# Kernel tuning notes

Hardware: AMD Instinct MI355X
Metric: run time of the kernel (lower is better)

The kernel has to match this reference:

```python
import jax, jax.numpy as jnp
import numpy as np

B, W, L, J, I, O = 512, 1024, 64, 8, 32, 128


def setup_inputs() -> dict:
    key = jax.random.key(0)
    ks = jax.random.split(key, 9)
    wm = jax.random.normal(ks[0], (B, W, L), dtype=jnp.float32)
    constants = jax.random.uniform(ks[1], (J, L), minval=-1.0, maxval=1.0, dtype=jnp.float32)
    gammas = jax.random.uniform(ks[2], (J, L), minval=0.0, maxval=1.0, dtype=jnp.float32)
    body_w = jax.random.normal(ks[3], (J, I, L), dtype=jnp.float32) / np.sqrt(L).astype(np.float32)
    body_b = jax.random.normal(ks[4], (J, I), dtype=jnp.float32) * 0.01
    slot_w = jax.random.normal(ks[5], (J, L * I, L), dtype=jnp.float32) / np.sqrt(L).astype(np.float32)
    slot_b = jax.random.normal(ks[6], (J, L * I), dtype=jnp.float32) * 0.01
    head_w = jax.random.normal(ks[7], (O, I), dtype=jnp.float32) / np.sqrt(I).astype(np.float32)
    head_b = jax.random.normal(ks[8], (O,), dtype=jnp.float32) * 0.01
    return {"working_memory": wm, "constants": constants, "gammas": gammas,
            "body_w": body_w, "body_b": body_b, "slot_w": slot_w, "slot_b": slot_b,
            "head_w": head_w, "head_b": head_b}


def reference(working_memory, constants, gammas, body_w, body_b, slot_w, slot_b, head_w, head_b):
    temperature = 1.0
    g = jnp.clip(gammas, 0.0, 1.0)            # (J,L), torch.clamp equivalent
    w1 = 1.0 - g                               # per-element weight (1-gamma)
    # match_scores[j,b,w] = sum_l w1[j,l] * (c[j,l] - wm[b,w,l])^2, expanded to
    # avoid materializing a (J,B,W,L) intermediate:
    A = jnp.sum(w1 * constants * constants, axis=1)                      # (J,)
    cross = jnp.einsum('jl,bwl->jbw', w1 * constants, working_memory)    # (J,B,W)
    quad = jnp.einsum('jl,bwl->jbw', w1, working_memory * working_memory)
    scores = A[:, None, None] - 2.0 * cross + quad                       # (J,B,W)
    attn = jax.nn.softmax(-scores / temperature, axis=-1)                # (J,B,W)
    best = jnp.einsum('jbw,bwl->jbl', attn, working_memory)              # (J,B,L)
    total_mq = jnp.sum(attn * scores, axis=-1).sum(axis=0)               # (B,)
    # body: per-premise Linear(L->I), scaled by mean clamped gamma
    captured = jnp.einsum('jbl,jil->jbi', best, body_w) + body_b[:, None, :]
    g_avg = g.mean(axis=1)                                               # (J,)
    captured_vars = jnp.einsum('j,jbi->bi', g_avg, captured)             # (B,I)
    # slot selector: per-premise Linear(L -> L*I), softmax over slots,
    # scatter best_props values into slots (the original inner l-loop).
    slot_logits = jnp.einsum('jbl,jkl->jbk', best, slot_w) + slot_b[:, None, :]
    slot_probs = jax.nn.softmax(slot_logits.reshape(J, -1, L, I), axis=-1)
    captured_vars = captured_vars + jnp.einsum('jbli,jbl->bi', slot_probs, best)
    output = captured_vars @ head_w.T + head_b                           # (B,O)
    confidence = jnp.exp(-total_mq)[:, None]                             # (B,1)
    return confidence * output
```

## Files before the change

### kernel.cpp

```cpp
#include <hip/hip_runtime.h>
#include <cstdint>
#include <cstddef>

#define B_ 512
#define W_ 1024
#define L_ 64
#define J_ 8
#define I_ 32
#define O_ 128


__global__ __launch_bounds__(64) void k0_prep(const float* __restrict__ constants,
    const float* __restrict__ gammas, float* __restrict__ wcg,
    float* __restrict__ w1g, float* __restrict__ Ag)
{
  const int l = threadIdx.x;
  #pragma unroll
  for (int j = 0; j < J_; ++j) {
    float g = gammas[j*L_ + l];
    g = fminf(fmaxf(g, 0.f), 1.f);
    float c = constants[j*L_ + l];
    float w1 = 1.f - g;
    w1g[j*L_ + l] = w1;
    wcg[j*L_ + l] = w1 * c;
  }
  if (l < J_) {
    float a = 0.f;
    for (int c = 0; c < L_; ++c) {
      float g = gammas[l*L_ + c];
      g = fminf(fmaxf(g, 0.f), 1.f);
      float cc = constants[l*L_ + c];
      a += (1.f - g) * cc * cc;
    }
    Ag[l] = a;
  }
}

__global__ __launch_bounds__(256, 4) void k12_fused(const float* __restrict__ wm,
    const float* __restrict__ wcg, const float* __restrict__ w1g,
    const float* __restrict__ Ag, float* __restrict__ bpart, float* __restrict__ stats)
{
  __shared__ __align__(16) float xs[128 * 68];
  __shared__ __align__(16) float es[J_ * 128];
  __shared__ float redA[4][4], redB[4][4];
  __shared__ float bcast[J_];

  const int tid = threadIdx.x;
  const int b = blockIdx.x, h = blockIdx.y;
  const int lane = tid & 63, wv = tid >> 6;
  const int w = tid & 127;
  const int jh = tid >> 7;
  const int jbase = __builtin_amdgcn_readfirstlane(jh << 2);
  const int lq = tid & 15, wsl = tid >> 4;

  float accb[J_][4];
  #pragma unroll
  for (int j = 0; j < J_; ++j)
    #pragma unroll
    for (int q = 0; q < 4; ++q) accb[j][q] = 0.f;
  float esum[4], msum[4], m0[4];
  #pragma unroll
  for (int jj = 0; jj < 4; ++jj) { esum[jj] = 0.f; msum[jj] = 0.f; }

  const float* wmb = wm + (size_t)b * (W_*L_) + (size_t)h * (512*L_);

  for (int ch = 0; ch < 4; ++ch) {
    __syncthreads();
    const float4* src = (const float4*)(wmb + ch * (128*L_));
    #pragma unroll
    for (int k = 0; k < 8; ++k) {
      int f = k*256 + tid;
      float4 v = src[f];
      int rw = f >> 4, lw = f & 15;
      *(float4*)&xs[rw*68 + lw*4] = v;
    }
    __syncthreads();

    float a1[4], a2[4];
    #pragma unroll
    for (int jj = 0; jj < 4; ++jj) { a1[jj] = 0.f; a2[jj] = 0.f; }
    #pragma unroll
    for (int c = 0; c < 16; ++c) {
      float4 x = *(const float4*)&xs[w*68 + c*4];
      float4 xq;
      xq.x = x.x*x.x; xq.y = x.y*x.y; xq.z = x.z*x.z; xq.w = x.w*x.w;
      #pragma unroll
      for (int jj = 0; jj < 4; ++jj) {
        float4 wc4 = *(const float4*)(wcg + (jbase+jj)*L_ + c*4);
        float4 w14 = *(const float4*)(w1g + (jbase+jj)*L_ + c*4);
        a1[jj] = fmaf(wc4.x, x.x, a1[jj]);
        a1[jj] = fmaf(wc4.y, x.y, a1[jj]);
        a1[jj] = fmaf(wc4.z, x.z, a1[jj]);
        a1[jj] = fmaf(wc4.w, x.w, a1[jj]);
        a2[jj] = fmaf(w14.x, xq.x, a2[jj]);
        a2[jj] = fmaf(w14.y, xq.y, a2[jj]);
        a2[jj] = fmaf(w14.z, xq.z, a2[jj]);
        a2[jj] = fmaf(w14.w, xq.w, a2[jj]);
      }
    }
    float s[4];
    #pragma unroll
    for (int jj = 0; jj < 4; ++jj)
      s[jj] = Ag[jbase+jj] - 2.f*a1[jj] + a2[jj];

    if (ch == 0) {
      #pragma unroll
      for (int jj = 0; jj < 4; ++jj) {
        float mn = s[jj];
        #pragma unroll
        for (int off = 1; off < 64; off <<= 1)
          mn = fminf(mn, __shfl_xor(mn, off));
        if (lane == 0) redA[wv][jj] = mn;
      }
      __syncthreads();
      if (tid < J_) {
        int jj = tid & 3;
        bcast[tid] = (tid < 4) ? fminf(redA[0][jj], redA[1][jj])
                               : fminf(redA[2][jj], redA[3][jj]);
      }
      __syncthreads();
      #pragma unroll
      for (int jj = 0; jj < 4; ++jj) m0[jj] = bcast[jbase+jj];
    }

    #pragma unroll
    for (int jj = 0; jj < 4; ++jj) {
      float e = __expf(m0[jj] - s[jj]);
      esum[jj] += e;
      msum[jj] = fmaf(e, s[jj], msum[jj]);
      es[(jbase+jj)*128 + w] = e;
    }
    __syncthreads();

    #pragma unroll
    for (int tg = 0; tg < 2; ++tg) {
      float4 e4[J_];
      #pragma unroll
      for (int j = 0; j < J_; ++j)
        e4[j] = *(const float4*)&es[j*128 + wsl*8 + tg*4];
      #pragma unroll
      for (int t = 0; t < 4; ++t) {
        int w2 = wsl*8 + tg*4 + t;
        float4 x = *(const float4*)&xs[w2*68 + lq*4];
        #pragma unroll
        for (int j = 0; j < J_; ++j) {
          float ej = (t == 0) ? e4[j].x : (t == 1) ? e4[j].y
                   : (t == 2) ? e4[j].z : e4[j].w;
          accb[j][0] = fmaf(ej, x.x, accb[j][0]);
          accb[j][1] = fmaf(ej, x.y, accb[j][1]);
          accb[j][2] = fmaf(ej, x.z, accb[j][2]);
          accb[j][3] = fmaf(ej, x.w, accb[j][3]);
        }
      }
    }
  }

  #pragma unroll
  for (int jj = 0; jj < 4; ++jj) {
    float e = esum[jj], m = msum[jj];
    #pragma unroll
    for (int off = 1; off < 64; off <<= 1) {
      e += __shfl_xor(e, off);
      m += __shfl_xor(m, off);
    }
    if (lane == 0) { redA[wv][jj] = e; redB[wv][jj] = m; }
  }
  __syncthreads();
  if (tid < J_) {
    int jj = tid & 3;
    float E = (tid < 4) ? redA[0][jj] + redA[1][jj] : redA[2][jj] + redA[3][jj];
    float M = (tid < 4) ? redB[0][jj] + redB[1][jj] : redB[2][jj] + redB[3][jj];
    float* st = stats + (((size_t)h*B_ + b)*J_ + tid)*4;
    st[0] = bcast[tid]; st[1] = E; st[2] = M;
  }

  #pragma unroll
  for (int j = 0; j < J_; ++j)
    *(float4*)&xs[((wsl*J_ + j)*16 + lq)*4] = *(float4*)accb[j];
  __syncthreads();
  if (tid < J_*16) {
    int j = tid >> 4, q = tid & 15;
    float4 sum = make_float4(0.f, 0.f, 0.f, 0.f);
    #pragma unroll
    for (int s2 = 0; s2 < 16; ++s2) {
      float4 p = *(const float4*)&xs[((s2*J_ + j)*16 + q)*4];
      sum.x += p.x; sum.y += p.y; sum.z += p.z; sum.w += p.w;
    }
    *(float4*)&bpart[(((size_t)h*J_ + j)*B_ + b)*L_ + q*4] = sum;
  }
}

__global__ __launch_bounds__(128) void k2b_combine(const float* __restrict__ bpart,
    const float* __restrict__ stats, float* __restrict__ best, float* __restrict__ conf)
{
  __shared__ float mred[J_];
  const int b = blockIdx.x, tid = threadIdx.x;
  const int j = tid >> 4, q = tid & 15;
  const float* st0 = stats + ((size_t)b*J_ + j)*4;
  const float* st1 = stats + (((size_t)B_ + b)*J_ + j)*4;
  float m0a = st0[0], E0 = st0[1], M0 = st0[2];
  float m0b = st1[0], E1 = st1[1], M1 = st1[2];
  float M = fminf(m0a, m0b);
  float s0 = __expf(M - m0a), s1 = __expf(M - m0b);
  float E = s0*E0 + s1*E1;
  float inv = 1.f / E;
  float4 p0 = *(const float4*)&bpart[((size_t)j*B_ + b)*L_ + q*4];
  float4 p1 = *(const float4*)&bpart[(((size_t)J_ + j)*B_ + b)*L_ + q*4];
  float4 o;
  o.x = (s0*p0.x + s1*p1.x) * inv;
  o.y = (s0*p0.y + s1*p1.y) * inv;
  o.z = (s0*p0.z + s1*p1.z) * inv;
  o.w = (s0*p0.w + s1*p1.w) * inv;
  *(float4*)&best[((size_t)j*B_ + b)*L_ + q*4] = o;
  if (q == 0) mred[j] = (s0*M0 + s1*M1) * inv;
  __syncthreads();
  if (tid == 0) {
    float mq = 0.f;
    #pragma unroll
    for (int jj = 0; jj < J_; ++jj) mq += mred[jj];
    conf[b] = __expf(-mq);
  }
}

__global__ __launch_bounds__(256) void k3_slot(const float* __restrict__ slot_w,
    const float* __restrict__ slot_b, const float* __restrict__ best,
    float* __restrict__ partial)
{
  const int bx = blockIdx.y;
  const int j = bx >> 3, lg = bx & 7;
  const int bc = blockIdx.x;
  const int tid = threadIdx.x;
  const int wv = tid >> 6, lane = tid & 63;
  const int l2 = lane >> 5, i = lane & 31;
  const int l = lg*8 + wv*2 + l2;
  const int r = l*I_ + i;

  const float* swr = slot_w + ((size_t)j*(L_*I_) + r) * L_;
  float sw[L_];
  #pragma unroll
  for (int c = 0; c < 16; ++c) {
    float4 t = ((const float4*)swr)[c];
    sw[c*4+0] = t.x; sw[c*4+1] = t.y; sw[c*4+2] = t.z; sw[c*4+3] = t.w;
  }
  const float sb = slot_b[j*(L_*I_) + r];
  const float* bestj = best + (size_t)j * B_ * L_;
  float* pout = partial + (size_t)bx * (B_*I_);
  const int lidx = lg*8 + wv*2;

  for (int bi = 0; bi < 32; bi += 2) {
    const int b0 = bc*32 + bi;
    const float* bw0 = bestj + (size_t)b0 * L_;
    const float* bw1 = bw0 + L_;
    float p00 = sb, p01 = 0.f, p02 = 0.f, p03 = 0.f;
    float p10 = sb, p11 = 0.f, p12 = 0.f, p13 = 0.f;
    #pragma unroll
    for (int c = 0; c < L_; c += 4) {
      p00 = fmaf(bw0[c+0], sw[c+0], p00);
      p10 = fmaf(bw1[c+0], sw[c+0], p10);
      p01 = fmaf(bw0[c+1], sw[c+1], p01);
      p11 = fmaf(bw1[c+1], sw[c+1], p11);
      p02 = fmaf(bw0[c+2], sw[c+2], p02);
      p12 = fmaf(bw1[c+2], sw[c+2], p12);
      p03 = fmaf(bw0[c+3], sw[c+3], p03);
      p13 = fmaf(bw1[c+3], sw[c+3], p13);
    }
    float lg0 = (p00 + p01) + (p02 + p03);
    float lg1 = (p10 + p11) + (p12 + p13);
    float m0v = lg0, m1v = lg1;
    #pragma unroll
    for (int mask = 16; mask; mask >>= 1) {
      m0v = fmaxf(m0v, __shfl_xor(m0v, mask));
      m1v = fmaxf(m1v, __shfl_xor(m1v, mask));
    }
    float e0 = __expf(lg0 - m0v), e1 = __expf(lg1 - m1v);
    float s0 = e0, s1 = e1;
    #pragma unroll
    for (int mask = 16; mask; mask >>= 1) {
      s0 += __shfl_xor(s0, mask);
      s1 += __shfl_xor(s1, mask);
    }
    float bv0 = l2 ? bw0[lidx+1] : bw0[lidx];
    float bv1 = l2 ? bw1[lidx+1] : bw1[lidx];
    float c0 = (e0 / s0) * bv0;
    float c1 = (e1 / s1) * bv1;
    c0 += __shfl_xor(c0, 32);
    c1 += __shfl_xor(c1, 32);
    if (l2 == 0) {
      pout[(size_t)b0*I_ + i] = c0;
      pout[(size_t)(b0+1)*I_ + i] = c1;
    }
  }
}

__global__ __launch_bounds__(128) void k4_head(const float* __restrict__ partial,
    const float* __restrict__ best, const float* __restrict__ gammas,
    const float* __restrict__ body_w, const float* __restrict__ body_b,
    const float* __restrict__ head_w, const float* __restrict__ head_b,
    const float* __restrict__ conf, float* __restrict__ out)
{
  __shared__ float gavg[J_];
  __shared__ float cvred[4][I_];
  __shared__ float cvf[I_];
  const int b = blockIdx.x, tid = threadIdx.x;
  if (tid < J_) {
    float gsum = 0.f;
    for (int l = 0; l < L_; ++l) {
      float g = gammas[tid*L_ + l];
      gsum += fminf(fmaxf(g, 0.f), 1.f);
    }
    gavg[tid] = gsum * (1.f / L_);
  }
  const int i = tid & 31, q = tid >> 5;
  float acc = 0.f;
  for (int s = q; s < 64; s += 4)
    acc += partial[((size_t)s*B_ + b)*I_ + i];
  cvred[q][i] = acc;
  __syncthreads();
  if (tid < I_) {
    float cv = cvred[0][i] + cvred[1][i] + cvred[2][i] + cvred[3][i];
    #pragma unroll
    for (int j = 0; j < J_; ++j) {
      const float* bw   = best + ((size_t)j*B_ + b)*L_;
      const float* wrow = body_w + (size_t)(j*I_ + i)*L_;
      float d = body_b[j*I_ + i];
      for (int c = 0; c < L_; ++c) d = fmaf(bw[c], wrow[c], d);
      cv += gavg[j] * d;
    }
    cvf[i] = cv;
  }
  __syncthreads();
  float oacc = head_b[tid];
  #pragma unroll
  for (int i2 = 0; i2 < I_; ++i2) oacc = fmaf(cvf[i2], head_w[tid*I_ + i2], oacc);
  out[(size_t)b*O_ + tid] = conf[b] * oacc;
}

extern "C" void kernel_launch(void* const* d_in, const int* in_sizes, int n_in,
                              void* d_out, int out_size, void* d_ws, size_t ws_size,
                              hipStream_t stream) {
  const float* wm        = (const float*)d_in[0];
  const float* constants = (const float*)d_in[1];
  const float* gammas    = (const float*)d_in[2];
  const float* body_w    = (const float*)d_in[3];
  const float* body_b    = (const float*)d_in[4];
  const float* slot_w    = (const float*)d_in[5];
  const float* slot_b    = (const float*)d_in[6];
  const float* head_w    = (const float*)d_in[7];
  const float* head_b    = (const float*)d_in[8];
  float* out = (float*)d_out;

  float* ws      = (float*)d_ws;
  float* wcg     = ws;
  float* w1g     = wcg + J_*L_;
  float* Ag      = w1g + J_*L_;
  float* best    = Ag + 16;
  float* conf    = best + (size_t)J_*B_*L_;
  float* partial = conf + B_;
  float* bpart   = partial + (size_t)64*B_*I_;
  float* stats   = bpart + (size_t)2*J_*B_*L_;

  hipLaunchKernelGGL(k0_prep, dim3(1), dim3(64), 0, stream,
                     constants, gammas, wcg, w1g, Ag);
  hipLaunchKernelGGL(k12_fused, dim3(B_, 2), dim3(256), 0, stream,
                     wm, wcg, w1g, Ag, bpart, stats);
  hipLaunchKernelGGL(k2b_combine, dim3(B_), dim3(128), 0, stream,
                     bpart, stats, best, conf);
  hipLaunchKernelGGL(k3_slot, dim3(16, 64), dim3(256), 0, stream,
                     slot_w, slot_b, best, partial);
  hipLaunchKernelGGL(k4_head, dim3(B_), dim3(128), 0, stream,
                     partial, best, gammas, body_w, body_b, head_w, head_b, conf, out);
}
```

Baseline: 311.0 us.

## Retune occupancy, reorder attention-weighted accumulate, unroll slot batches, parallelize head body

Relaxes the k12 launch bound from 4 to 2 waves per SIMD so the compiler has more registers. It also reorders the weighted-sum loop to preload four x rows and stream one es float4 per j. The slot kernel now handles four batch rows per iteration instead of two to get more ILP per sw register load. The head kernel spreads the body projection over all 128 threads instead of 32, at the cost of an extra barrier.

```diff
diff --git a/kernel.cpp b/kernel.cpp
--- a/kernel.cpp
+++ b/kernel.cpp
@@ -36,7 +36,7 @@
   }
 }
 
-__global__ __launch_bounds__(256, 4) void k12_fused(const float* __restrict__ wm,
+__global__ __launch_bounds__(256, 2) void k12_fused(const float* __restrict__ wm,
     const float* __restrict__ wcg, const float* __restrict__ w1g,
     const float* __restrict__ Ag, float* __restrict__ bpart, float* __restrict__ stats)
 {
@@ -134,23 +134,29 @@
 
     #pragma unroll
     for (int tg = 0; tg < 2; ++tg) {
-      float4 e4[J_];
-      #pragma unroll
-      for (int j = 0; j < J_; ++j)
-        e4[j] = *(const float4*)&es[j*128 + wsl*8 + tg*4];
-      #pragma unroll
-      for (int t = 0; t < 4; ++t) {
-        int w2 = wsl*8 + tg*4 + t;
-        float4 x = *(const float4*)&xs[w2*68 + lq*4];
-        #pragma unroll
-        for (int j = 0; j < J_; ++j) {
-          float ej = (t == 0) ? e4[j].x : (t == 1) ? e4[j].y
-                   : (t == 2) ? e4[j].z : e4[j].w;
-          accb[j][0] = fmaf(ej, x.x, accb[j][0]);
-          accb[j][1] = fmaf(ej, x.y, accb[j][1]);
-          accb[j][2] = fmaf(ej, x.z, accb[j][2]);
-          accb[j][3] = fmaf(ej, x.w, accb[j][3]);
-        }
+      float4 x[4];
+      #pragma unroll
+      for (int t = 0; t < 4; ++t)
+        x[t] = *(const float4*)&xs[(wsl*8 + tg*4 + t)*68 + lq*4];
+      #pragma unroll
+      for (int j = 0; j < J_; ++j) {
+        float4 e4 = *(const float4*)&es[j*128 + wsl*8 + tg*4];
+        accb[j][0] = fmaf(e4.x, x[0].x, accb[j][0]);
+        accb[j][1] = fmaf(e4.x, x[0].y, accb[j][1]);
+        accb[j][2] = fmaf(e4.x, x[0].z, accb[j][2]);
+        accb[j][3] = fmaf(e4.x, x[0].w, accb[j][3]);
+        accb[j][0] = fmaf(e4.y, x[1].x, accb[j][0]);
+        accb[j][1] = fmaf(e4.y, x[1].y, accb[j][1]);
+        accb[j][2] = fmaf(e4.y, x[1].z, accb[j][2]);
+        accb[j][3] = fmaf(e4.y, x[1].w, accb[j][3]);
+        accb[j][0] = fmaf(e4.z, x[2].x, accb[j][0]);
+        accb[j][1] = fmaf(e4.z, x[2].y, accb[j][1]);
+        accb[j][2] = fmaf(e4.z, x[2].z, accb[j][2]);
+        accb[j][3] = fmaf(e4.z, x[2].w, accb[j][3]);
+        accb[j][0] = fmaf(e4.w, x[3].x, accb[j][0]);
+        accb[j][1] = fmaf(e4.w, x[3].y, accb[j][1]);
+        accb[j][2] = fmaf(e4.w, x[3].z, accb[j][2]);
+        accb[j][3] = fmaf(e4.w, x[3].w, accb[j][3]);
       }
     }
   }
@@ -247,47 +253,47 @@
   float* pout = partial + (size_t)bx * (B_*I_);
   const int lidx = lg*8 + wv*2;
 
-  for (int bi = 0; bi < 32; bi += 2) {
+  for (int bi = 0; bi < 32; bi += 4) {
     const int b0 = bc*32 + bi;
-    const float* bw0 = bestj + (size_t)b0 * L_;
-    const float* bw1 = bw0 + L_;
-    float p00 = sb, p01 = 0.f, p02 = 0.f, p03 = 0.f;
-    float p10 = sb, p11 = 0.f, p12 = 0.f, p13 = 0.f;
-    #pragma unroll
-    for (int c = 0; c < L_; c += 4) {
-      p00 = fmaf(bw0[c+0], sw[c+0], p00);
-      p10 = fmaf(bw1[c+0], sw[c+0], p10);
-      p01 = fmaf(bw0[c+1], sw[c+1], p01);
-      p11 = fmaf(bw1[c+1], sw[c+1], p11);
-      p02 = fmaf(bw0[c+2], sw[c+2], p02);
-      p12 = fmaf(bw1[c+2], sw[c+2], p12);
-      p03 = fmaf(bw0[c+3], sw[c+3], p03);
-      p13 = fmaf(bw1[c+3], sw[c+3], p13);
-    }
-    float lg0 = (p00 + p01) + (p02 + p03);
-    float lg1 = (p10 + p11) + (p12 + p13);
-    float m0v = lg0, m1v = lg1;
-    #pragma unroll
-    for (int mask = 16; mask; mask >>= 1) {
-      m0v = fmaxf(m0v, __shfl_xor(m0v, mask));
-      m1v = fmaxf(m1v, __shfl_xor(m1v, mask));
-    }
-    float e0 = __expf(lg0 - m0v), e1 = __expf(lg1 - m1v);
-    float s0 = e0, s1 = e1;
-    #pragma unroll
-    for (int mask = 16; mask; mask >>= 1) {
-      s0 += __shfl_xor(s0, mask);
-      s1 += __shfl_xor(s1, mask);
-    }
-    float bv0 = l2 ? bw0[lidx+1] : bw0[lidx];
-    float bv1 = l2 ? bw1[lidx+1] : bw1[lidx];
-    float c0 = (e0 / s0) * bv0;
-    float c1 = (e1 / s1) * bv1;
-    c0 += __shfl_xor(c0, 32);
-    c1 += __shfl_xor(c1, 32);
+    const float* bw[4];
+    #pragma unroll
+    for (int u = 0; u < 4; ++u) bw[u] = bestj + (size_t)(b0+u) * L_;
+    float pa[4], pb[4];
+    #pragma unroll
+    for (int u = 0; u < 4; ++u) { pa[u] = sb; pb[u] = 0.f; }
+    #pragma unroll
+    for (int c = 0; c < L_; c += 2) {
+      #pragma unroll
+      for (int u = 0; u < 4; ++u) {
+        pa[u] = fmaf(bw[u][c+0], sw[c+0], pa[u]);
+        pb[u] = fmaf(bw[u][c+1], sw[c+1], pb[u]);
+      }
+    }
+    float lgt[4], mx[4], e[4], sm[4];
+    #pragma unroll
+    for (int u = 0; u < 4; ++u) { lgt[u] = pa[u] + pb[u]; mx[u] = lgt[u]; }
+    #pragma unroll
+    for (int mask = 16; mask; mask >>= 1)
+      #pragma unroll
+      for (int u = 0; u < 4; ++u) mx[u] = fmaxf(mx[u], __shfl_xor(mx[u], mask));
+    #pragma unroll
+    for (int u = 0; u < 4; ++u) { e[u] = __expf(lgt[u] - mx[u]); sm[u] = e[u]; }
+    #pragma unroll
+    for (int mask = 16; mask; mask >>= 1)
+      #pragma unroll
+      for (int u = 0; u < 4; ++u) sm[u] += __shfl_xor(sm[u], mask);
+    float cv[4];
+    #pragma unroll
+    for (int u = 0; u < 4; ++u) {
+      float bv = l2 ? bw[u][lidx+1] : bw[u][lidx];
+      cv[u] = (e[u] / sm[u]) * bv;
+    }
+    #pragma unroll
+    for (int u = 0; u < 4; ++u) cv[u] += __shfl_xor(cv[u], 32);
     if (l2 == 0) {
-      pout[(size_t)b0*I_ + i] = c0;
-      pout[(size_t)(b0+1)*I_ + i] = c1;
+      #pragma unroll
+      for (int u = 0; u < 4; ++u)
+        pout[(size_t)(b0+u)*I_ + i] = cv[u];
     }
   }
 }
@@ -302,6 +308,7 @@
   __shared__ float cvred[4][I_];
   __shared__ float cvf[I_];
   const int b = blockIdx.x, tid = threadIdx.x;
+  const int i = tid & 31, q = tid >> 5;
   if (tid < J_) {
     float gsum = 0.f;
     for (int l = 0; l < L_; ++l) {
@@ -310,24 +317,31 @@
     }
     gavg[tid] = gsum * (1.f / L_);
   }
-  const int i = tid & 31, q = tid >> 5;
+  __syncthreads();
+
   float acc = 0.f;
   for (int s = q; s < 64; s += 4)
     acc += partial[((size_t)s*B_ + b)*I_ + i];
+
+  #pragma unroll
+  for (int u = 0; u < 2; ++u) {
+    const int j = q + u*4;
+    const float* bwv  = best + ((size_t)j*B_ + b)*L_;
+    const float* wrow = body_w + (size_t)(j*I_ + i)*L_;
+    float d0 = body_b[j*I_ + i], d1 = 0.f, d2 = 0.f, d3 = 0.f;
+    #pragma unroll
+    for (int c = 0; c < L_; c += 4) {
+      d0 = fmaf(bwv[c+0], wrow[c+0], d0);
+      d1 = fmaf(bwv[c+1], wrow[c+1], d1);
+      d2 = fmaf(bwv[c+2], wrow[c+2], d2);
+      d3 = fmaf(bwv[c+3], wrow[c+3], d3);
+    }
+    acc = fmaf(gavg[j], (d0 + d1) + (d2 + d3), acc);
+  }
   cvred[q][i] = acc;
   __syncthreads();
-  if (tid < I_) {
-    float cv = cvred[0][i] + cvred[1][i] + cvred[2][i] + cvred[3][i];
-    #pragma unroll
-    for (int j = 0; j < J_; ++j) {
-      const float* bw   = best + ((size_t)j*B_ + b)*L_;
-      const float* wrow = body_w + (size_t)(j*I_ + i)*L_;
-      float d = body_b[j*I_ + i];
-      for (int c = 0; c < L_; ++c) d = fmaf(bw[c], wrow[c], d);
-      cv += gavg[j] * d;
-    }
-    cvf[i] = cv;
-  }
+  if (tid < I_)
+    cvf[i] = cvred[0][i] + cvred[1][i] + cvred[2][i] + cvred[3][i];
   __syncthreads();
   float oacc = head_b[tid];
   #pragma unroll
```

After: 289.1 us. 7.0% less time.
